# Kernel optimization log

Hardware: AMD Instinct MI355X
Metric: run time of the kernel (lower is better)

The kernel has to match this reference:

```python
import jax, jax.numpy as jnp
import numpy as np

G, S, D = 2, 1024, 2048   # dispatch_group_size, seq_len_per_chip, hidden_dim
E, K = 8, 2               # num_routed_experts, num_experts_per_tok


def setup_inputs() -> dict:
    key = jax.random.key(0)
    ks = jax.random.split(key, 10)
    scale = 1.0 / np.sqrt(D)
    return {
        "x": jax.random.normal(ks[0], (G, S, D), jnp.float32),
        "weights": jax.random.uniform(ks[1], (G, S, K), jnp.float32),
        "indices": jax.random.randint(ks[2], (G, S, K), 0, E, jnp.int64),
        "expert_offsets": jnp.zeros((G, E), jnp.int64),
        "expert_token_counts": jnp.zeros((G, E), jnp.int64),
        # routed expert weights stacked over experts; F.linear(x, W) = x @ W.T, W is [out,in]=[D,D]
        "gate_w": jax.random.normal(ks[3], (E, D, D), jnp.float32) * scale,
        "up_w": jax.random.normal(ks[4], (E, D, D), jnp.float32) * scale,
        "down_w": jax.random.normal(ks[5], (E, D, D), jnp.float32) * scale,
        "shared_gate_w": jax.random.normal(ks[6], (D, D), jnp.float32) * scale,
        "shared_up_w": jax.random.normal(ks[7], (D, D), jnpp_dummy) if False else jax.random.normal(ks[7], (D, D), jnp.float32) * scale,
        "shared_down_w": jax.random.normal(ks[8], (D, D), jnp.float32) * scale,
    }


def expert_ffn(x, gw, uw, dw):
    # SiLU-gated FFN: silu(x @ gw.T) * (x @ uw.T) @ dw.T
    gate = jnp.einsum("gsd,od->gso", x, gw)
    up = jnp.einsum("gsd,od->gso", x, uw)
    act = jax.nn.silu(gate) * up
    return jnp.einsum("gsa,oa->gso", act, dw)


def reference(x, weights, indices, expert_offsets, expert_token_counts,
              gate_w, up_w, down_w, shared_gate_w, shared_up_w, shared_down_w):
    x = x.astype(jnp.float32)
    # shared expert on original tokens
    shared_out = expert_ffn(x, shared_gate_w, shared_up_w, shared_down_w)  # [G,S,D]

    # routed experts: compute all E expert FFNs densely (small E), then gather top-k
    gate = jnp.einsum("gsd,eod->egso", x, gate_w)      # [E,G,S,D]
    up = jnp.einsum("gsd,eod->egso", x, up_w)
    act = jax.nn.silu(gate) * up
    all_out = jnp.einsum("egsa,eoa->egso", act, down_w)  # [E,G,S,D]

    per_tok = jnp.transpose(all_out, (1, 2, 0, 3))       # [G,S,E,D]
    combined = jnp.take_along_axis(per_tok, indices[..., None], axis=2)  # [G,S,K,D]
    routed_out = jnp.sum(combined * weights[..., None], axis=2)          # [G,S,D]

    return routed_out + shared_out
```

## Files before the change

### kernel.cpp

```cpp
#include <hip/hip_runtime.h>
#include <cstdint>
#include <cstddef>

#define DHID 2048
#define NEXP 8
#define NTOK 2048
#define NPAIR 4096
#define NROWS 6144
#define MAXTILES 55
#define DD ((size_t)DHID * DHID)

typedef __attribute__((ext_vector_type(8))) __bf16 bf16x8;
typedef __attribute__((ext_vector_type(4))) float f32x4;

typedef __attribute__((address_space(3))) void lds_void;
typedef __attribute__((address_space(1))) void gbl_void;

__device__ __forceinline__ void gload16(const void* g, void* l) {
  __builtin_amdgcn_global_load_lds((gbl_void*)g, (lds_void*)l, 16, 0, 0);
}

__global__ void route_kernel(const int* __restrict__ idx, const float* __restrict__ wts,
                             int* __restrict__ tok_id, float* __restrict__ tok_w,
                             int* __restrict__ dst_id,
                             int* __restrict__ cnts, int* __restrict__ offs,
                             int2* __restrict__ tiles) {
  __shared__ int c[NEXP];
  __shared__ int cur[NEXP];
  const int t = threadIdx.x;
  if (t < NEXP) c[t] = 0;
  __syncthreads();
  for (int p = t; p < NPAIR; p += 256) atomicAdd(&c[idx[p]], 1);
  __syncthreads();
  if (t == 0) {
    int run = 0;
    for (int e = 0; e < NEXP; ++e) { cur[e] = run; offs[e] = run; cnts[e] = c[e]; run += c[e]; }
    offs[NEXP] = NPAIR; cnts[NEXP] = NTOK;
    int nt = 0;
    for (int e = 0; e <= NEXP; ++e) {
      const int ce = (e < NEXP) ? c[e] : NTOK;
      for (int m0 = 0; m0 < ce; m0 += 128) { tiles[nt].x = e; tiles[nt].y = m0; ++nt; }
    }
    for (; nt < MAXTILES; ++nt) { tiles[nt].x = -1; tiles[nt].y = 0; }
  }
  __syncthreads();
  for (int p = t; p < NPAIR; p += 256) {
    const int e = idx[p];
    const int slot = atomicAdd(&cur[e], 1);
    tok_id[slot] = p >> 1;
    tok_w[slot] = wts[p];
    dst_id[slot] = p;
  }
  for (int i = t; i < NTOK; i += 256) {
    tok_id[NPAIR + i] = i; tok_w[NPAIR + i] = 1.0f; dst_id[NPAIR + i] = NPAIR + i;
  }
}

__global__ void cast_all_kernel(const float4* __restrict__ gw, const float4* __restrict__ sgw,
                                const float4* __restrict__ uw, const float4* __restrict__ suw,
                                const float4* __restrict__ dwn, const float4* __restrict__ sdw,
                                const float4* __restrict__ x, bf16x8* __restrict__ dst) {
  const size_t L = DD / 8;
  const size_t i = (size_t)blockIdx.x * 256 + threadIdx.x;
  size_t r = i;
  const float4* src;
  if (r < 8 * L) { src = gw; }
  else if ((r -= 8 * L) < L) { src = sgw; }
  else if ((r -= L) < 8 * L) { src = uw; }
  else if ((r -= 8 * L) < L) { src = suw; }
  else if ((r -= L) < 8 * L) { src = dwn; }
  else if ((r -= 8 * L) < L) { src = sdw; }
  else { r -= L; src = x; }
  const float4 a = src[2 * r];
  const float4 b = src[2 * r + 1];
  bf16x8 o;
  o[0] = (__bf16)a.x; o[1] = (__bf16)a.y; o[2] = (__bf16)a.z; o[3] = (__bf16)a.w;
  o[4] = (__bf16)b.x; o[5] = (__bf16)b.y; o[6] = (__bf16)b.z; o[7] = (__bf16)b.w;
  dst[i] = o;
}

__global__ __launch_bounds__(256, 3) void gateup_kernel(
    const __bf16* __restrict__ xb,
    const __bf16* __restrict__ wbg, const __bf16* __restrict__ wbu,
    __bf16* __restrict__ act,
    const int* __restrict__ tok_id,
    const int* __restrict__ cnts, const int* __restrict__ offs,
    const int2* __restrict__ tiles) {
  const int2 tl = tiles[blockIdx.y];
  const int e = tl.x;
  if (e < 0) return;
  const int m0 = tl.y;
  const int cnt = cnts[e];
  const int n0 = blockIdx.x * 64;
  const int off = offs[e];
  const __bf16* Bg = wbg + (size_t)e * DD;
  const __bf16* Bu = wbu + (size_t)e * DD;

  __shared__ __align__(16) char sA[128 * 64 * 2];
  __shared__ __align__(16) char sBg[64 * 64 * 2];
  __shared__ __align__(16) char sBu[64 * 64 * 2];

  const int tid = threadIdx.x;
  const int lane = tid & 63;
  const int wv = tid >> 6;
  const int mw = (wv >> 1) * 64;
  const int nw = (wv & 1) * 32;
  const int q4 = lane >> 4;
  const int ln = lane & 15;

  const int rbase = tid >> 3;
  const int part = (tid & 7) ^ (rbase & 7);

  const char* gA[4];
#pragma unroll
  for (int j = 0; j < 4; ++j) {
    int r = m0 + rbase + 32 * j;
    r = (r < cnt) ? r : (cnt - 1);
    gA[j] = (const char*)(xb + (size_t)tok_id[off + r] * DHID) + part * 16;
  }
  const char* gBg[2]; const char* gBu[2];
#pragma unroll
  for (int j = 0; j < 2; ++j) {
    gBg[j] = (const char*)(Bg + (size_t)(n0 + rbase + 32 * j) * DHID) + part * 16;
    gBu[j] = (const char*)(Bu + (size_t)(n0 + rbase + 32 * j) * DHID) + part * 16;
  }

  f32x4 accg[4][2], accu[4][2];
  const f32x4 vz = {0.f, 0.f, 0.f, 0.f};
#pragma unroll
  for (int i = 0; i < 4; ++i)
#pragma unroll
    for (int j = 0; j < 2; ++j) { accg[i][j] = vz; accu[i][j] = vz; }

  for (int kt = 0; kt < DHID; kt += 64) {
#pragma unroll
    for (int j = 0; j < 4; ++j)
      gload16(gA[j] + (size_t)kt * 2, sA + (tid + j * 256) * 16);
#pragma unroll
    for (int j = 0; j < 2; ++j) {
      gload16(gBg[j] + (size_t)kt * 2, sBg + (tid + j * 256) * 16);
      gload16(gBu[j] + (size_t)kt * 2, sBu + (tid + j * 256) * 16);
    }
    __syncthreads();

#pragma unroll
    for (int h = 0; h < 2; ++h) {
      bf16x8 af[4];
#pragma unroll
      for (int im = 0; im < 4; ++im) {
        const int r = mw + im * 16 + ln;
        af[im] = *(const bf16x8*)(sA + ((r * 8 + ((q4 + 4 * h) ^ (r & 7))) << 4));
      }
#pragma unroll
      for (int in_ = 0; in_ < 2; ++in_) {
        const int r = nw + in_ * 16 + ln;
        const int c = (r * 8 + ((q4 + 4 * h) ^ (r & 7))) << 4;
        const bf16x8 bg = *(const bf16x8*)(sBg + c);
        const bf16x8 bu = *(const bf16x8*)(sBu + c);
#pragma unroll
        for (int im = 0; im < 4; ++im) {
          accg[im][in_] = __builtin_amdgcn_mfma_f32_16x16x32_bf16(af[im], bg, accg[im][in_], 0, 0, 0);
          accu[im][in_] = __builtin_amdgcn_mfma_f32_16x16x32_bf16(af[im], bu, accu[im][in_], 0, 0, 0);
        }
      }
    }
    __syncthreads();
  }

#pragma unroll
  for (int im = 0; im < 4; ++im) {
#pragma unroll
    for (int rr = 0; rr < 4; ++rr) {
      const int row = mw + im * 16 + q4 * 4 + rr;
      if (m0 + row < cnt) {
        __bf16* dst = act + (size_t)(off + m0 + row) * DHID + n0 + nw + ln;
#pragma unroll
        for (int in_ = 0; in_ < 2; ++in_) {
          const float gg = accg[im][in_][rr];
          const float uu = accu[im][in_][rr];
          const float a = (gg / (1.0f + __expf(-gg))) * uu;
          dst[in_ * 16] = (__bf16)a;
        }
      }
    }
  }
}

__global__ __launch_bounds__(256, 3) void down_kernel(
    const __bf16* __restrict__ act,
    const __bf16* __restrict__ wbd,
    float* __restrict__ buf,
    const float* __restrict__ tok_w, const int* __restrict__ dst_id,
    const int* __restrict__ cnts, const int* __restrict__ offs,
    const int2* __restrict__ tiles) {
  const int2 tl = tiles[blockIdx.y];
  const int e = tl.x;
  if (e < 0) return;
  const int m0 = tl.y;
  const int cnt = cnts[e];
  const int n0 = blockIdx.x * 64;
  const int off = offs[e];
  const __bf16* B = wbd + (size_t)e * DD;

  __shared__ __align__(16) char sA[128 * 64 * 2];
  __shared__ __align__(16) char sB[64 * 64 * 2];

  const int tid = threadIdx.x;
  const int lane = tid & 63;
  const int wv = tid >> 6;
  const int mw = (wv >> 1) * 64;
  const int nw = (wv & 1) * 32;
  const int q4 = lane >> 4;
  const int ln = lane & 15;

  const int rbase = tid >> 3;
  const int part = (tid & 7) ^ (rbase & 7);

  const char* gA[4];
#pragma unroll
  for (int j = 0; j < 4; ++j)
    gA[j] = (const char*)(act + (size_t)(off + m0 + rbase + 32 * j) * DHID) + part * 16;
  const char* gB[2];
#pragma unroll
  for (int j = 0; j < 2; ++j)
    gB[j] = (const char*)(B + (size_t)(n0 + rbase + 32 * j) * DHID) + part * 16;

  f32x4 acc[4][2];
  const f32x4 vz = {0.f, 0.f, 0.f, 0.f};
#pragma unroll
  for (int i = 0; i < 4; ++i)
#pragma unroll
    for (int j = 0; j < 2; ++j) acc[i][j] = vz;

  for (int kt = 0; kt < DHID; kt += 64) {
#pragma unroll
    for (int j = 0; j < 4; ++j)
      gload16(gA[j] + (size_t)kt * 2, sA + (tid + j * 256) * 16);
#pragma unroll
    for (int j = 0; j < 2; ++j)
      gload16(gB[j] + (size_t)kt * 2, sB + (tid + j * 256) * 16);
    __syncthreads();

#pragma unroll
    for (int h = 0; h < 2; ++h) {
      bf16x8 af[4];
#pragma unroll
      for (int im = 0; im < 4; ++im) {
        const int r = mw + im * 16 + ln;
        af[im] = *(const bf16x8*)(sA + ((r * 8 + ((q4 + 4 * h) ^ (r & 7))) << 4));
      }
#pragma unroll
      for (int in_ = 0; in_ < 2; ++in_) {
        const int r = nw + in_ * 16 + ln;
        const bf16x8 bb = *(const bf16x8*)(sB + ((r * 8 + ((q4 + 4 * h) ^ (r & 7))) << 4));
#pragma unroll
        for (int im = 0; im < 4; ++im)
          acc[im][in_] = __builtin_amdgcn_mfma_f32_16x16x32_bf16(af[im], bb, acc[im][in_], 0, 0, 0);
      }
    }
    __syncthreads();
  }

#pragma unroll
  for (int im = 0; im < 4; ++im) {
#pragma unroll
    for (int rr = 0; rr < 4; ++rr) {
      const int row = mw + im * 16 + q4 * 4 + rr;
      if (m0 + row < cnt) {
        const int gr = off + m0 + row;
        const float wt = tok_w[gr];
        float* dst = buf + (size_t)dst_id[gr] * DHID + n0 + nw + ln;
#pragma unroll
        for (int in_ = 0; in_ < 2; ++in_)
          dst[in_ * 16] = wt * acc[im][in_][rr];
      }
    }
  }
}

__global__ void combine_kernel(const float4* __restrict__ buf, float4* __restrict__ out) {
  const int i = blockIdx.x * 256 + threadIdx.x;
  const int t = i >> 9;
  const int d = i & 511;
  const float4 a = buf[(size_t)(2 * t) * 512 + d];
  const float4 b = buf[(size_t)(2 * t + 1) * 512 + d];
  const float4 c = buf[(size_t)(NPAIR + t) * 512 + d];
  float4 r;
  r.x = a.x + b.x + c.x; r.y = a.y + b.y + c.y;
  r.z = a.z + b.z + c.z; r.w = a.w + b.w + c.w;
  out[i] = r;
}

extern "C" void kernel_launch(void* const* d_in, const int* in_sizes, int n_in,
                              void* d_out, int out_size, void* d_ws, size_t ws_size,
                              hipStream_t stream) {
  (void)in_sizes; (void)n_in; (void)out_size; (void)ws_size;
  const float* x   = (const float*)d_in[0];
  const float* wts = (const float*)d_in[1];
  const int*   idx = (const int*)d_in[2];
  const float* gw  = (const float*)d_in[5];
  const float* uw  = (const float*)d_in[6];
  const float* dwn = (const float*)d_in[7];
  const float* sgw = (const float*)d_in[8];
  const float* suw = (const float*)d_in[9];
  const float* sdw = (const float*)d_in[10];
  float* out = (float*)d_out;
  char* ws = (char*)d_ws;

  const size_t WB    = 3 * 9 * DD * 2;
  const size_t XBsz  = (size_t)NTOK * DHID * 2;
  const size_t ACTsz = (size_t)NROWS * DHID * 2;
  const size_t BUFsz = (size_t)NROWS * DHID * 4;

  __bf16* wbg = (__bf16*)ws;
  __bf16* wbu = wbg + 9 * DD;
  __bf16* wbd = wbu + 9 * DD;
  __bf16* xb  = (__bf16*)(ws + WB);
  __bf16* act = (__bf16*)(ws + WB + XBsz);
  float*  buf = (float*)(ws + WB + XBsz + ACTsz);
  char*   rt  = ws + WB + XBsz + ACTsz + BUFsz;
  int*   tok_id = (int*)rt;
  float* tok_w  = (float*)(rt + NROWS * 4);
  int*   dst_id = (int*)(rt + NROWS * 8);
  int*   cnts   = (int*)(rt + NROWS * 12);
  int*   offs   = cnts + 16;
  int2*  tiles  = (int2*)(offs + 16);

  route_kernel<<<1, 256, 0, stream>>>(idx, wts, tok_id, tok_w, dst_id, cnts, offs, tiles);
  cast_all_kernel<<<57344, 256, 0, stream>>>((const float4*)gw, (const float4*)sgw,
                                             (const float4*)uw, (const float4*)suw,
                                             (const float4*)dwn, (const float4*)sdw,
                                             (const float4*)x, (bf16x8*)ws);
  gateup_kernel<<<dim3(32, MAXTILES), 256, 0, stream>>>(
      xb, wbg, wbu, act, tok_id, cnts, offs, tiles);
  down_kernel<<<dim3(32, MAXTILES), 256, 0, stream>>>(
      act, wbd, buf, tok_w, dst_id, cnts, offs, tiles);
  combine_kernel<<<4096, 256, 0, stream>>>((const float4*)buf, (float4*)out);
}
```

Baseline: 659.1 us.

## Widen down-proj tile to 128 columns and coalesce fp32-to-bf16 cast with nontemporal loads

```diff
diff --git a/kernel.cpp b/kernel.cpp
--- a/kernel.cpp
+++ b/kernel.cpp
@@ -11,6 +11,7 @@
 #define DD ((size_t)DHID * DHID)
 
 typedef __attribute__((ext_vector_type(8))) __bf16 bf16x8;
+typedef __attribute__((ext_vector_type(4))) __bf16 bf16x4;
 typedef __attribute__((ext_vector_type(4))) float f32x4;
 
 typedef __attribute__((address_space(3))) void lds_void;
@@ -56,27 +57,29 @@
   }
 }
 
-__global__ void cast_all_kernel(const float4* __restrict__ gw, const float4* __restrict__ sgw,
-                                const float4* __restrict__ uw, const float4* __restrict__ suw,
-                                const float4* __restrict__ dwn, const float4* __restrict__ sdw,
-                                const float4* __restrict__ x, bf16x8* __restrict__ dst) {
-  const size_t L = DD / 8;
-  const size_t i = (size_t)blockIdx.x * 256 + threadIdx.x;
-  size_t r = i;
-  const float4* src;
-  if (r < 8 * L) { src = gw; }
-  else if ((r -= 8 * L) < L) { src = sgw; }
-  else if ((r -= L) < 8 * L) { src = uw; }
-  else if ((r -= 8 * L) < L) { src = suw; }
-  else if ((r -= L) < 8 * L) { src = dwn; }
-  else if ((r -= 8 * L) < L) { src = sdw; }
-  else { r -= L; src = x; }
-  const float4 a = src[2 * r];
-  const float4 b = src[2 * r + 1];
-  bf16x8 o;
-  o[0] = (__bf16)a.x; o[1] = (__bf16)a.y; o[2] = (__bf16)a.z; o[3] = (__bf16)a.w;
-  o[4] = (__bf16)b.x; o[5] = (__bf16)b.y; o[6] = (__bf16)b.z; o[7] = (__bf16)b.w;
-  dst[i] = o;
+__global__ void cast_all_kernel(const f32x4* __restrict__ gw, const f32x4* __restrict__ sgw,
+                                const f32x4* __restrict__ uw, const f32x4* __restrict__ suw,
+                                const f32x4* __restrict__ dwn, const f32x4* __restrict__ sdw,
+                                const f32x4* __restrict__ x, bf16x4* __restrict__ dst) {
+  const size_t L4 = DD / 4;
+  const size_t base = (size_t)blockIdx.x * 512 + threadIdx.x;
+#pragma unroll
+  for (int half = 0; half < 2; ++half) {
+    const size_t f = base + (size_t)half * 256;
+    size_t r = f;
+    const f32x4* src;
+    if (r < 8 * L4) { src = gw; }
+    else if ((r -= 8 * L4) < L4) { src = sgw; }
+    else if ((r -= L4) < 8 * L4) { src = uw; }
+    else if ((r -= 8 * L4) < L4) { src = suw; }
+    else if ((r -= L4) < 8 * L4) { src = dwn; }
+    else if ((r -= 8 * L4) < L4) { src = sdw; }
+    else { r -= L4; src = x; }
+    const f32x4 a = __builtin_nontemporal_load(src + r);
+    bf16x4 o;
+    o[0] = (__bf16)a[0]; o[1] = (__bf16)a[1]; o[2] = (__bf16)a[2]; o[3] = (__bf16)a[3];
+    dst[f] = o;
+  }
 }
 
 __global__ __launch_bounds__(256, 3) void gateup_kernel(
@@ -198,18 +201,18 @@
   if (e < 0) return;
   const int m0 = tl.y;
   const int cnt = cnts[e];
-  const int n0 = blockIdx.x * 64;
+  const int n0 = blockIdx.x * 128;
   const int off = offs[e];
   const __bf16* B = wbd + (size_t)e * DD;
 
   __shared__ __align__(16) char sA[128 * 64 * 2];
-  __shared__ __align__(16) char sB[64 * 64 * 2];
+  __shared__ __align__(16) char sB[128 * 64 * 2];
 
   const int tid = threadIdx.x;
   const int lane = tid & 63;
   const int wv = tid >> 6;
   const int mw = (wv >> 1) * 64;
-  const int nw = (wv & 1) * 32;
+  const int nw = (wv & 1) * 64;
   const int q4 = lane >> 4;
   const int ln = lane & 15;
 
@@ -217,46 +220,46 @@
   const int part = (tid & 7) ^ (rbase & 7);
 
   const char* gA[4];
-#pragma unroll
-  for (int j = 0; j < 4; ++j)
+  const char* gB[4];
+#pragma unroll
+  for (int j = 0; j < 4; ++j) {
     gA[j] = (const char*)(act + (size_t)(off + m0 + rbase + 32 * j) * DHID) + part * 16;
-  const char* gB[2];
-#pragma unroll
-  for (int j = 0; j < 2; ++j)
     gB[j] = (const char*)(B + (size_t)(n0 + rbase + 32 * j) * DHID) + part * 16;
-
-  f32x4 acc[4][2];
+  }
+
+  f32x4 acc[4][4];
   const f32x4 vz = {0.f, 0.f, 0.f, 0.f};
 #pragma unroll
   for (int i = 0; i < 4; ++i)
 #pragma unroll
-    for (int j = 0; j < 2; ++j) acc[i][j] = vz;
+    for (int j = 0; j < 4; ++j) acc[i][j] = vz;
 
   for (int kt = 0; kt < DHID; kt += 64) {
 #pragma unroll
-    for (int j = 0; j < 4; ++j)
+    for (int j = 0; j < 4; ++j) {
       gload16(gA[j] + (size_t)kt * 2, sA + (tid + j * 256) * 16);
-#pragma unroll
-    for (int j = 0; j < 2; ++j)
       gload16(gB[j] + (size_t)kt * 2, sB + (tid + j * 256) * 16);
+    }
     __syncthreads();
 
 #pragma unroll
     for (int h = 0; h < 2; ++h) {
-      bf16x8 af[4];
+      bf16x8 af[4], bfr[4];
 #pragma unroll
       for (int im = 0; im < 4; ++im) {
         const int r = mw + im * 16 + ln;
         af[im] = *(const bf16x8*)(sA + ((r * 8 + ((q4 + 4 * h) ^ (r & 7))) << 4));
       }
 #pragma unroll
-      for (int in_ = 0; in_ < 2; ++in_) {
+      for (int in_ = 0; in_ < 4; ++in_) {
         const int r = nw + in_ * 16 + ln;
-        const bf16x8 bb = *(const bf16x8*)(sB + ((r * 8 + ((q4 + 4 * h) ^ (r & 7))) << 4));
+        bfr[in_] = *(const bf16x8*)(sB + ((r * 8 + ((q4 + 4 * h) ^ (r & 7))) << 4));
+      }
+#pragma unroll
+      for (int in_ = 0; in_ < 4; ++in_)
 #pragma unroll
         for (int im = 0; im < 4; ++im)
-          acc[im][in_] = __builtin_amdgcn_mfma_f32_16x16x32_bf16(af[im], bb, acc[im][in_], 0, 0, 0);
-      }
+          acc[im][in_] = __builtin_amdgcn_mfma_f32_16x16x32_bf16(af[im], bfr[in_], acc[im][in_], 0, 0, 0);
     }
     __syncthreads();
   }
@@ -271,7 +274,7 @@
         const float wt = tok_w[gr];
         float* dst = buf + (size_t)dst_id[gr] * DHID + n0 + nw + ln;
 #pragma unroll
-        for (int in_ = 0; in_ < 2; ++in_)
+        for (int in_ = 0; in_ < 4; ++in_)
           dst[in_ * 16] = wt * acc[im][in_][rr];
       }
     }
@@ -327,13 +330,13 @@
   int2*  tiles  = (int2*)(offs + 16);
 
   route_kernel<<<1, 256, 0, stream>>>(idx, wts, tok_id, tok_w, dst_id, cnts, offs, tiles);
-  cast_all_kernel<<<57344, 256, 0, stream>>>((const float4*)gw, (const float4*)sgw,
-                                             (const float4*)uw, (const float4*)suw,
-                                             (const float4*)dwn, (const float4*)sdw,
-                                             (const float4*)x, (bf16x8*)ws);
+  cast_all_kernel<<<57344, 256, 0, stream>>>((const f32x4*)gw, (const f32x4*)sgw,
+                                             (const f32x4*)uw, (const f32x4*)suw,
+                                             (const f32x4*)dwn, (const f32x4*)sdw,
+                                             (const f32x4*)x, (bf16x4*)ws);
   gateup_kernel<<<dim3(32, MAXTILES), 256, 0, stream>>>(
       xb, wbg, wbu, act, tok_id, cnts, offs, tiles);
-  down_kernel<<<dim3(32, MAXTILES), 256, 0, stream>>>(
+  down_kernel<<<dim3(16, MAXTILES), 256, 0, stream>>>(
       act, wbd, buf, tok_w, dst_id, cnts, offs, tiles);
   combine_kernel<<<4096, 256, 0, stream>>>((const float4*)buf, (float4*)out);
 }
```

New measurement: 608.0 us. 1.08x faster.
